# Kernel optimization log

Hardware: AMD Instinct MI355X
Metric: run time of the kernel (lower is better)

## Reference

```python
import jax, jax.numpy as jnp
import numpy as np

DIM = 512
HEADS = 16
HEAD_DIM = DIM // HEADS
WH, WW = 7, 7
N = WH * WW
OUP = 512
SCALE = HEAD_DIM ** -0.5
NW = 64  # windows per image (mask leading dim)


def _relative_position_index():
    coords = np.stack(np.meshgrid(np.arange(WH), np.arange(WW), indexing='ij'))  # (2,Wh,Ww)
    flat = coords.reshape(2, -1)                           # (2, N)
    rel = flat[:, :, None] - flat[:, None, :]              # (2, N, N)
    rel = rel.transpose(1, 2, 0).astype(np.int64)          # (N, N, 2)
    rel[:, :, 0] += WH - 1
    rel[:, :, 1] += WW - 1
    rel[:, :, 0] *= 2 * WW - 1
    return jnp.asarray(rel.sum(-1))                        # (N, N) int

REL_IDX = _relative_position_index()


def setup_inputs() -> dict:
    key = jax.random.key(0)
    ks = jax.random.split(key, 8)
    B_ = 4096
    x = jax.random.normal(ks[0], (B_, N, DIM), dtype=jnp.float32)
    mask = jnp.zeros((NW, N, N), dtype=jnp.float32)
    qkv_w = jax.random.normal(ks[1], (3 * DIM, DIM), dtype=jnp.float32) * (DIM ** -0.5)
    qkv_b = jax.random.normal(ks[2], (3 * DIM,), dtype=jnp.float32) * 0.02
    table = jax.random.normal(ks[3], ((2 * WH - 1) * (2 * WW - 1), HEADS), dtype=jnp.float32) * 0.02
    proj_w = jax.random.normal(ks[4], (OUP, DIM), dtype=jnp.float32) * (DIM ** -0.5)
    proj_b = jax.random.normal(ks[5], (OUP,), dtype=jnp.float32) * 0.02
    return {"x": x, "mask": mask, "qkv_w": qkv_w, "qkv_b": qkv_b,
            "table": table, "proj_w": proj_w, "proj_b": proj_b}


def reference(x, mask, qkv_w, qkv_b, table, proj_w, proj_b):
    B_, n, c = x.shape
    qkv = x @ qkv_w.T + qkv_b                               # (B_, N, 3C)
    qkv = qkv.reshape(B_, n, 3, HEADS, HEAD_DIM).transpose(2, 0, 3, 1, 4)
    q, k, v = qkv[0], qkv[1], qkv[2]                        # (B_, H, N, hd)
    q = q * SCALE
    attn = jnp.einsum('bhnd,bhmd->bhnm', q, k)              # (B_, H, N, N)
    bias = table[REL_IDX]                                   # (N, N, H) gather
    attn = attn + bias.transpose(2, 0, 1)[None]             # add rel-pos bias
    nW = mask.shape[0]
    attn = attn.reshape(B_ // nW, nW, HEADS, n, n) + mask[None, :, None]
    attn = attn.reshape(B_, HEADS, n, n)
    attn = jax.nn.softmax(attn, axis=-1)
    out = jnp.einsum('bhnm,bhmd->bhnd', attn, v)            # (B_, H, N, hd)
    out = out.transpose(0, 2, 1, 3).reshape(B_, n, c)
    return out @ proj_w.T + proj_b
```

## Files before the change

kernel.cpp:

```cpp
#include <hip/hip_runtime.h>
#include <hip/hip_bf16.h>
#include <stdint.h>

#define DIMC 512
#define HEADS 16
#define HEAD_DIM 32
#define NTOK 49
#define SCALE 0.17677669529663687f
#define LOG2E 1.4426950408889634f
#define MTOK 200704

typedef unsigned short u16;
typedef short bf16x8 __attribute__((ext_vector_type(8)));
typedef float f32x4 __attribute__((ext_vector_type(4)));
typedef u16 u16x4 __attribute__((ext_vector_type(4)));
typedef u16 u16x8 __attribute__((ext_vector_type(8)));

#define MFMA16(a, b, c) __builtin_amdgcn_mfma_f32_16x16x32_bf16((a), (b), (c), 0, 0, 0)

__device__ __forceinline__ u16 f2bf(float f) {
  __hip_bfloat16 h = __float2bfloat16(f);
  u16 u;
  __builtin_memcpy(&u, &h, 2);
  return u;
}

__device__ __forceinline__ float bf2f(u16 u) {
  const uint32_t b = ((uint32_t)u) << 16;
  float f;
  __builtin_memcpy(&f, &b, 4);
  return f;
}

__device__ __forceinline__ void gld16(const void* g, void* l) {
  __builtin_amdgcn_global_load_lds(
      (const __attribute__((address_space(1))) uint32_t*)g,
      (__attribute__((address_space(3))) uint32_t*)l, 16, 0, 0);
}

__global__ void cvt_f32_bf16(const float* __restrict__ in, u16* __restrict__ out, int n) {
  const int stride = gridDim.x * blockDim.x;
  for (int i = blockIdx.x * blockDim.x + threadIdx.x; i * 8 < n; i += stride) {
    const float4 v0 = ((const float4*)(in + i * 8))[0];
    const float4 v1 = ((const float4*)(in + i * 8))[1];
    u16x8 r;
    r[0] = f2bf(v0.x); r[1] = f2bf(v0.y); r[2] = f2bf(v0.z); r[3] = f2bf(v0.w);
    r[4] = f2bf(v1.x); r[5] = f2bf(v1.y); r[6] = f2bf(v1.z); r[7] = f2bf(v1.w);
    *(u16x8*)(out + i * 8) = r;
  }
}

__global__ void biasmask_kernel(const float* __restrict__ table, const float* __restrict__ mask,
                                u16* __restrict__ bm) {
  const int wm = blockIdx.x >> 4;
  const int h  = blockIdx.x & 15;
  for (int e = threadIdx.x; e < 4096; e += 256) {
    const int r = e & 3, lane = (e >> 2) & 63, fj = (e >> 8) & 3, fi = e >> 10;
    const int qrow = fi * 16 + (lane & 15);
    const int kcol = fj * 16 + (lane >> 4) * 4 + r;
    float v;
    if (qrow < NTOK && kcol < NTOK) {
      const int yi = qrow / 7, xi = qrow % 7, yj = kcol / 7, xj = kcol % 7;
      const int idx = (yi - yj + 6) * 13 + (xi - xj + 6);
      v = (table[idx * HEADS + h] + mask[wm * (NTOK * NTOK) + qrow * NTOK + kcol]) * LOG2E;
    } else {
      v = -1e30f;
    }
    bm[(size_t)blockIdx.x * 4096 + e] = f2bf(v);
  }
}

template<bool OUT_BF16, bool HEADMAJOR_C, bool A_HEADMAJOR>
__global__ void gemm_bf16(const u16* __restrict__ Ap, const u16* __restrict__ Bp,
                          const float* __restrict__ bias, void* __restrict__ Cp,
                          int M, int N, int K, int nxt) {
  __shared__ u16 As[128 * 64];
  __shared__ u16 Bs[128 * 64];
  const int t = threadIdx.x;
  const int lane = t & 63;
  const int q = gridDim.x >> 3;
  const int lin = blockIdx.x;
  const int l = (lin & 7) * q + (lin >> 3);
  const int bm0 = (l / nxt) * 128;
  const int bn0 = (l % nxt) * 128;
  const int wv = t >> 6, wr = wv >> 1, wc = wv & 1;
  const int lr = lane & 15, lg = lane >> 4;

  f32x4 acc[4][4] = {};

  int soff[4];
#pragma unroll
  for (int k = 0; k < 4; ++k) {
    const int c = t + 256 * k;
    const int row = c >> 3, sub = c & 7;
    soff[k] = ((sub ^ (row & 7)) * 8);
  }

  const int nK = K >> 6;
  for (int kt = 0; kt < nK; ++kt) {
    const int k0 = kt << 6;
    __syncthreads();
#pragma unroll
    for (int k = 0; k < 4; ++k) {
      const int c = t + 256 * k;
      const int row = c >> 3;
      if (A_HEADMAJOR) {
        const int col0 = k0 + soff[k];
        gld16(Ap + ((size_t)(col0 >> 5) * MTOK + bm0 + row) * 32 + (col0 & 31),
              As + c * 8);
      } else {
        gld16(Ap + (size_t)(bm0 + row) * K + k0 + soff[k], As + c * 8);
      }
      gld16(Bp + (size_t)(bn0 + row) * K + k0 + soff[k], Bs + c * 8);
    }
    __syncthreads();

#pragma unroll
    for (int kk = 0; kk < 2; ++kk) {
      bf16x8 af[4], bfr[4];
#pragma unroll
      for (int i = 0; i < 4; ++i) {
        const int row = wr * 64 + i * 16 + lr;
        af[i] = *(const bf16x8*)&As[row * 64 + (((kk * 4 + lg) ^ (row & 7)) << 3)];
      }
#pragma unroll
      for (int j = 0; j < 4; ++j) {
        const int row = wc * 64 + j * 16 + lr;
        bfr[j] = *(const bf16x8*)&Bs[row * 64 + (((kk * 4 + lg) ^ (row & 7)) << 3)];
      }
#pragma unroll
      for (int i = 0; i < 4; ++i)
#pragma unroll
        for (int j = 0; j < 4; ++j)
          acc[i][j] = MFMA16(af[i], bfr[j], acc[i][j]);
    }
  }

#pragma unroll
  for (int j = 0; j < 4; ++j) {
    const int col = bn0 + wc * 64 + j * 16 + lr;
    const float bv = bias[col];
    const int p = col >> 9, hh = (col & 511) >> 5, d = col & 31;
    const float sc = (HEADMAJOR_C && p == 0) ? SCALE * LOG2E : 1.0f;
#pragma unroll
    for (int i = 0; i < 4; ++i) {
      const int row0 = bm0 + wr * 64 + i * 16 + lg * 4;
#pragma unroll
      for (int r = 0; r < 4; ++r) {
        const float val = (acc[i][j][r] + bv) * sc;
        if (HEADMAJOR_C) {
          ((u16*)Cp)[((size_t)hh * MTOK + row0 + r) * 96 + p * 32 + d] = f2bf(val);
        } else if (OUT_BF16) {
          ((u16*)Cp)[(size_t)(row0 + r) * N + col] = f2bf(val);
        } else {
          ((float*)Cp)[(size_t)(row0 + r) * N + col] = val;
        }
      }
    }
  }
}

__launch_bounds__(256, 4)
__global__ void attn_win(const u16* __restrict__ qkv, const u16* __restrict__ bmfrag,
                         u16* __restrict__ aout) {
  __shared__ u16 P[4][64 * 64];
  const int t = threadIdx.x, lane = t & 63, wv = t >> 6;
  const int lr = lane & 15, lg = lane >> 4;
  const int w = blockIdx.x >> 2;
  const int h = ((blockIdx.x & 3) << 2) + wv;
  const size_t baseh = ((size_t)h * MTOK + (size_t)w * NTOK) * 96;

  const u16* bmp = bmfrag + (((size_t)(w & 63) * 16 + h) << 12);
  f32x4 s[4][4];
#pragma unroll
  for (int i = 0; i < 4; ++i)
#pragma unroll
    for (int j = 0; j < 4; ++j) {
      const u16x4 b4 = *(const u16x4*)&bmp[((i * 4 + j) * 64 + lane) * 4];
#pragma unroll
      for (int r = 0; r < 4; ++r) s[i][j][r] = bf2f(b4[r]);
    }

  const bf16x8 zf = {};
  bf16x8 qf[4], kf[4];
#pragma unroll
  for (int i = 0; i < 4; ++i) {
    const int row = i * 16 + lr;
    const size_t roff = baseh + (size_t)row * 96 + lg * 8;
    qf[i] = (row < NTOK) ? *(const bf16x8*)&qkv[roff] : zf;
    kf[i] = (row < NTOK) ? *(const bf16x8*)&qkv[roff + 32] : zf;
  }

  __builtin_amdgcn_s_setprio(1);
#pragma unroll
  for (int i = 0; i < 4; ++i)
#pragma unroll
    for (int j = 0; j < 4; ++j)
      s[i][j] = MFMA16(kf[j], qf[i], s[i][j]);
  __builtin_amdgcn_s_setprio(0);

  bf16x8 vf[2][2];
#pragma unroll
  for (int ks = 0; ks < 2; ++ks)
#pragma unroll
    for (int dn = 0; dn < 2; ++dn)
#pragma unroll
      for (int e = 0; e < 8; ++e) {
        int kk = ks * 32 + lg * 8 + e;
        kk = kk < NTOK ? kk : 0;
        vf[ks][dn][e] = (short)qkv[baseh + (size_t)kk * 96 + 64 + dn * 16 + lr];
      }

  u16* Pw = &P[wv][0];
#pragma unroll
  for (int i = 0; i < 4; ++i)
#pragma unroll
    for (int j = 0; j < 4; ++j) {
      u16x4 pk;
#pragma unroll
      for (int r = 0; r < 4; ++r)
        pk[r] = f2bf(__builtin_amdgcn_exp2f(s[i][j][r]));
      *(u16x4*)&Pw[(i * 16 + lr) * 64 + (((j * 4 + lg) ^ (lr & 14)) << 2)] = pk;
    }

  bf16x8 ones;
#pragma unroll
  for (int e = 0; e < 8; ++e) ones[e] = (short)0x3F80;
  f32x4 o[4][2] = {};
  f32x4 osum[4] = {};
#pragma unroll
  for (int ks = 0; ks < 2; ++ks) {
    __builtin_amdgcn_s_setprio(1);
#pragma unroll
    for (int i = 0; i < 4; ++i) {
      const bf16x8 pa = *(const bf16x8*)
          &Pw[(i * 16 + lr) * 64 + (((ks * 8 + lg * 2) ^ (lr & 14)) << 2)];
#pragma unroll
      for (int dn = 0; dn < 2; ++dn)
        o[i][dn] = MFMA16(pa, vf[ks][dn], o[i][dn]);
      osum[i] = MFMA16(pa, ones, osum[i]);
    }
    __builtin_amdgcn_s_setprio(0);
  }

#pragma unroll
  for (int i = 0; i < 4; ++i)
#pragma unroll
    for (int r = 0; r < 4; ++r) {
      const int row = i * 16 + lg * 4 + r;
      if (row < NTOK) {
        const float rinv = __builtin_amdgcn_rcpf(osum[i][r]);
        const size_t ob = ((size_t)h * MTOK + (size_t)w * NTOK + row) * 32;
#pragma unroll
        for (int dn = 0; dn < 2; ++dn)
          aout[ob + dn * 16 + lr] = f2bf(o[i][dn][r] * rinv);
      }
    }
}

extern "C" void kernel_launch(void* const* d_in, const int* in_sizes, int n_in,
                              void* d_out, int out_size, void* d_ws, size_t ws_size,
                              hipStream_t stream) {
  const float* x      = (const float*)d_in[0];
  const float* mask   = (const float*)d_in[1];
  const float* qkv_w  = (const float*)d_in[2];
  const float* qkv_b  = (const float*)d_in[3];
  const float* table  = (const float*)d_in[4];
  const float* proj_w = (const float*)d_in[5];
  const float* proj_b = (const float*)d_in[6];
  float* out = (float*)d_out;

  const int M = MTOK;

  char* ws = (char*)d_ws;
  u16*   qkv_bf   = (u16*)ws;
  u16*   wqkv_bf  = (u16*)(ws + 616562688ull);
  u16*   wproj_bf = (u16*)(ws + 618135552ull);
  u16*   biasmask = (u16*)(ws + 618659840ull);
  u16*   x_bf     = (u16*)(ws + 627048448ull);
  u16*   attn_bf  = x_bf;

  cvt_f32_bf16<<<768, 256, 0, stream>>>(qkv_w, wqkv_bf, 1536 * 512);
  cvt_f32_bf16<<<256, 256, 0, stream>>>(proj_w, wproj_bf, 512 * 512);
  biasmask_kernel<<<1024, 256, 0, stream>>>(table, mask, biasmask);
  cvt_f32_bf16<<<1792, 256, 0, stream>>>(x, x_bf, M * DIMC);

  gemm_bf16<true, true, false><<<1568 * 12, 256, 0, stream>>>(
      x_bf, wqkv_bf, qkv_b, qkv_bf, M, 1536, 512, 12);

  attn_win<<<4096 * 4, 256, 0, stream>>>(qkv_bf, biasmask, attn_bf);

  gemm_bf16<false, false, true><<<1568 * 4, 256, 0, stream>>>(
      attn_bf, wproj_bf, proj_b, out, M, 512, 512, 4);
}
```

Measured before the change: 966.1 us.

## Double-buffer GEMM shared-memory tiles with BK=32 to overlap loads and MFMA

Converts the GEMM main loop from a single 128x64 LDS tile with two barriers per step to two 128x32 buffers. The next k-tile's global loads are issued before the current tile's MFMAs, leaving one barrier per step. This aims to hide global-load latency behind compute. In exchange, each step does half the MFMA work and so runs twice as many iterations, which may expose latency if the asynchronous loads are not actually overlapped.

```diff
diff --git a/kernel.cpp b/kernel.cpp
--- a/kernel.cpp
+++ b/kernel.cpp
@@ -74,8 +74,8 @@
 __global__ void gemm_bf16(const u16* __restrict__ Ap, const u16* __restrict__ Bp,
                           const float* __restrict__ bias, void* __restrict__ Cp,
                           int M, int N, int K, int nxt) {
-  __shared__ u16 As[128 * 64];
-  __shared__ u16 Bs[128 * 64];
+  __shared__ u16 As[2][128 * 32];
+  __shared__ u16 Bs[2][128 * 32];
   const int t = threadIdx.x;
   const int lane = t & 63;
   const int q = gridDim.x >> 3;
@@ -88,53 +88,59 @@
 
   f32x4 acc[4][4] = {};
 
-  int soff[4];
-#pragma unroll
-  for (int k = 0; k < 4; ++k) {
+  int srow[2], scol[2];
+#pragma unroll
+  for (int k = 0; k < 2; ++k) {
     const int c = t + 256 * k;
-    const int row = c >> 3, sub = c & 7;
-    soff[k] = ((sub ^ (row & 7)) * 8);
-  }
-
-  const int nK = K >> 6;
+    srow[k] = c >> 2;
+    scol[k] = ((c & 3) ^ (srow[k] & 3)) * 8;
+  }
+
+#define STAGE(KT, B)                                                             \
+  {                                                                              \
+    const int k0_ = (KT) << 5;                                                   \
+    _Pragma("unroll")                                                            \
+    for (int k = 0; k < 2; ++k) {                                                \
+      const int c = t + 256 * k;                                                 \
+      if (A_HEADMAJOR) {                                                         \
+        const int col0 = k0_ + scol[k];  \
+        gld16(Ap + ((size_t)(col0 >> 5) * MTOK + bm0 + srow[k]) * 32 + (col0 & 31), \
+              &As[B][c * 8]);                                                    \
+      } else {                                                                   \
+        gld16(Ap + (size_t)(bm0 + srow[k]) * K + k0_ + scol[k], &As[B][c * 8]);  \
+      }                                                                          \
+      gld16(Bp + (size_t)(bn0 + srow[k]) * K + k0_ + scol[k], &Bs[B][c * 8]);    \
+    }                                                                            \
+  }
+
+  STAGE(0, 0);
+  __syncthreads();
+
+  const int nK = K >> 5;
   for (int kt = 0; kt < nK; ++kt) {
-    const int k0 = kt << 6;
+    const int b = kt & 1;
+    if (kt + 1 < nK) STAGE(kt + 1, b ^ 1);
+
+    bf16x8 af[4], bfr[4];
+#pragma unroll
+    for (int i = 0; i < 4; ++i) {
+      const int row = wr * 64 + i * 16 + lr;
+      af[i] = *(const bf16x8*)&As[b][row * 32 + ((lg ^ (row & 3)) << 3)];
+    }
+#pragma unroll
+    for (int j = 0; j < 4; ++j) {
+      const int row = wc * 64 + j * 16 + lr;
+      bfr[j] = *(const bf16x8*)&Bs[b][row * 32 + ((lg ^ (row & 3)) << 3)];
+    }
+#pragma unroll
+    for (int i = 0; i < 4; ++i)
+#pragma unroll
+      for (int j = 0; j < 4; ++j)
+        acc[i][j] = MFMA16(af[i], bfr[j], acc[i][j]);
+
     __syncthreads();
-#pragma unroll
-    for (int k = 0; k < 4; ++k) {
-      const int c = t + 256 * k;
-      const int row = c >> 3;
-      if (A_HEADMAJOR) {
-        const int col0 = k0 + soff[k];
-        gld16(Ap + ((size_t)(col0 >> 5) * MTOK + bm0 + row) * 32 + (col0 & 31),
-              As + c * 8);
-      } else {
-        gld16(Ap + (size_t)(bm0 + row) * K + k0 + soff[k], As + c * 8);
-      }
-      gld16(Bp + (size_t)(bn0 + row) * K + k0 + soff[k], Bs + c * 8);
-    }
-    __syncthreads();
-
-#pragma unroll
-    for (int kk = 0; kk < 2; ++kk) {
-      bf16x8 af[4], bfr[4];
-#pragma unroll
-      for (int i = 0; i < 4; ++i) {
-        const int row = wr * 64 + i * 16 + lr;
-        af[i] = *(const bf16x8*)&As[row * 64 + (((kk * 4 + lg) ^ (row & 7)) << 3)];
-      }
-#pragma unroll
-      for (int j = 0; j < 4; ++j) {
-        const int row = wc * 64 + j * 16 + lr;
-        bfr[j] = *(const bf16x8*)&Bs[row * 64 + (((kk * 4 + lg) ^ (row & 7)) << 3)];
-      }
-#pragma unroll
-      for (int i = 0; i < 4; ++i)
-#pragma unroll
-        for (int j = 0; j < 4; ++j)
-          acc[i][j] = MFMA16(af[i], bfr[j], acc[i][j]);
-    }
-  }
+  }
+#undef STAGE
 
 #pragma unroll
   for (int j = 0; j < 4; ++j) {
```

Result: slower. 1.034 ms (+7.1%).
